# Optimization experiments

Hardware: AMD Instinct MI355X
Metric: run time of the kernel (lower is better)

Reference implementation:

```python
import jax, jax.numpy as jnp
import numpy as np

B, S, D, H = 2, 2048, 1024, 16
HD = D // H  # head dim = 64

def setup_inputs() -> dict:
    key = jax.random.key(0)
    ks = jax.random.split(key, 11)
    s = 0.02
    return {
        "query": jax.random.normal(ks[0], (B, S, D), jnp.float32),
        "key_in": jax.random.normal(ks[1], (B, S, D), jnp.float32),
        "value": jax.random.normal(ks[2], (B, S, D), jnp.float32),
        "Wq": jax.random.normal(ks[3], (D, D), jnp.float32) * s,
        "bq": jnp.zeros((D,), jnp.float32),
        "Wk": jax.random.normal(ks[4], (D, D), jnp.float32) * s,
        "bk": jnp.zeros((D,), jnp.float32),
        "Wv": jax.random.normal(ks[5], (D, D), jnp.float32) * s,
        "bv": jnp.zeros((D,), jnp.float32),
        "Wo": jax.random.normal(ks[6], (D, D), jnp.float32) * s,
        "bo": jnp.zeros((D,), jnp.float32),
    }

def _split_heads(x):
    b, s, _ = x.shape
    return x.reshape(b, s, H, HD).transpose(0, 2, 1, 3)  # [B,H,S,HD]

def reference(query, key_in, value, Wq, bq, Wk, bk, Wv, bv, Wo, bo):
    q = _split_heads(query @ Wq + bq)
    k = _split_heads(key_in @ Wk + bk)
    v = _split_heads(value @ Wv + bv)
    scores = jnp.einsum("bhqd,bhkd->bhqk", q, k) / jnp.sqrt(jnp.float32(HD))
    weights = jax.nn.softmax(scores, axis=-1)  # dropout = identity (eval)
    ctx = jnp.einsum("bhqk,bhkd->bhqd", weights, v)
    ctx = ctx.transpose(0, 2, 1, 3).reshape(query.shape[0], -1, D)
    return ctx @ Wo + bo
```

## Files before the change

kernel.cpp:

```cpp
#include <hip/hip_runtime.h>
#include <hip/hip_bf16.h>


typedef __attribute__((ext_vector_type(8))) short short8;
typedef __attribute__((ext_vector_type(4))) short short4v;
typedef __attribute__((ext_vector_type(4))) float f32x4;

static __device__ __forceinline__ short f2bf(float f) {
    union { float f; unsigned u; } c; c.f = f;
    unsigned r = c.u + 0x7fff + ((c.u >> 16) & 1);
    return (short)(r >> 16);
}

static __device__ __forceinline__ unsigned pk_bf16(float a, float b) {
    union { __hip_bfloat162 h; unsigned u; } c;
    c.h = __float22bfloat162_rn(make_float2(a, b));
    return c.u;
}

typedef const void __attribute__((address_space(1)))* gas_ptr;
typedef void __attribute__((address_space(3)))* las_ptr;
static __device__ __forceinline__ void gload16(const void* g, void* l) {
    __builtin_amdgcn_global_load_lds((gas_ptr)g, (las_ptr)l, 16, 0, 0);
}

__global__ __launch_bounds__(256) void prep(
    const float* __restrict__ X0, const float* __restrict__ X1,
    const float* __restrict__ X2, short* __restrict__ Abf,
    const float* __restrict__ W0, const float* __restrict__ W1,
    const float* __restrict__ W2, const float* __restrict__ W3,
    short* __restrict__ Wt)
{
    __shared__ float tile[32][33];
    const int bid = blockIdx.x;
    if (bid < 6144) {
        const int zz = bid >> 11, xb = bid & 2047;
        const float* X = zz == 0 ? X0 : zz == 1 ? X1 : X2;
        short* o = Abf + ((size_t)zz << 22);
        const int i = (xb * 256 + threadIdx.x) * 8;
        const float4 a = *(const float4*)(X + i);
        const float4 b = *(const float4*)(X + i + 4);
        uint4 r;
        r.x = pk_bf16(a.x, a.y); r.y = pk_bf16(a.z, a.w);
        r.z = pk_bf16(b.x, b.y); r.w = pk_bf16(b.z, b.w);
        *(uint4*)(o + i) = r;
    } else {
        const int wid = bid - 6144;
        const int z = wid >> 10;
        const float* W = z == 0 ? W0 : z == 1 ? W1 : z == 2 ? W2 : W3;
        short* O = Wt + ((size_t)z << 20);
        const int k0 = (wid & 31) * 32, n0 = ((wid >> 5) & 31) * 32;
        const int tx = threadIdx.x & 31, ty = threadIdx.x >> 5;
        #pragma unroll
        for (int j = 0; j < 32; j += 8)
            tile[ty + j][tx] = W[(k0 + ty + j) * 1024 + n0 + tx];
        __syncthreads();
        #pragma unroll
        for (int j = 0; j < 32; j += 8)
            O[(n0 + ty + j) * 1024 + k0 + tx] = f2bf(tile[tx][ty + j]);
    }
}

#define GEMM_CORE(Aa, Ba)                                                     \
    __shared__ short Al[2][2048];                           \
    __shared__ short Bl[2][4096];                          \
    const int t = threadIdx.x;                                                \
    const int m0 = blockIdx.y * 64, n0 = blockIdx.x * 128;                    \
    const int lane = t & 63, w = t >> 6;                                      \
    const int lm = lane & 15, lg = lane >> 4;                                 \
    const int wr = w >> 1, wc = w & 1;                                        \
    f32x4 acc[2][4] = {};                                                     \
    STAGE(0, 0);                                                              \
    __syncthreads();                                                          \
    int buf = 0;                                                              \
    for (int kk = 0; kk < 32; ++kk) {                                         \
        if (kk < 31) STAGE(buf ^ 1, (kk + 1) * 32);                           \
        const short* Ab = Al[buf];                                            \
        const short* Bb = Bl[buf];                                            \
        short8 af[2], bfr[4];                                                 \
        _Pragma("unroll")                                                     \
        for (int mf = 0; mf < 2; ++mf)                                        \
            af[mf] = *(const short8*)(Ab + (wr * 32 + mf * 16 + lm) * 32 + lg * 8); \
        _Pragma("unroll")                                                     \
        for (int nf = 0; nf < 4; ++nf)                                        \
            bfr[nf] = *(const short8*)(Bb + (wc * 64 + nf * 16 + lm) * 32 + lg * 8); \
        _Pragma("unroll")                                                     \
        for (int mf = 0; mf < 2; ++mf)                                        \
            _Pragma("unroll")                                                 \
            for (int nf = 0; nf < 4; ++nf)                                    \
                acc[mf][nf] = __builtin_amdgcn_mfma_f32_16x16x32_bf16(        \
                    af[mf], bfr[nf], acc[mf][nf], 0, 0, 0);                   \
        __syncthreads();                                                      \
        buf ^= 1;                                                             \
    }

#define STAGE(buf, k0) do {                                                   \
    gload16(Aa + (size_t)(m0 + (t >> 2)) * 1024 + (k0) + (t & 3) * 8,         \
            &Al[buf][w * 512]);                                               \
    _Pragma("unroll")                                                         \
    for (int j = 0; j < 2; ++j) {                                             \
        const int c = j * 256 + t;                                            \
        gload16(Ba + (size_t)(n0 + (c >> 2)) * 1024 + (k0) + (c & 3) * 8,     \
                &Bl[buf][j * 2048 + w * 512]);                                \
    }                                                                         \
} while (0)

__global__ __launch_bounds__(256) void gemmqkv(
    const short* __restrict__ Abase, const short* __restrict__ Wt,
    const float* __restrict__ bq, const float* __restrict__ bk,
    const float* __restrict__ bv, short* __restrict__ Qh,
    short* __restrict__ Kh, short* __restrict__ Vt, float qscale)
{
    const int z = blockIdx.z;
    const short* Aa = Abase + ((size_t)z << 22);
    const short* Ba = Wt + ((size_t)z << 20);
    const float* bias = z == 0 ? bq : z == 1 ? bk : bv;
    short* O = z == 0 ? Qh : z == 1 ? Kh : Vt;
    const float scale = z == 0 ? qscale : 1.0f;

    GEMM_CORE(Aa, Ba)

    #pragma unroll
    for (int mf = 0; mf < 2; ++mf) {
        const int mb = m0 + wr * 32 + mf * 16 + lg * 4;
        #pragma unroll
        for (int nf = 0; nf < 4; ++nf) {
            const int n = n0 + wc * 64 + nf * 16 + lm;
            const float bs = bias[n];
            if (z == 2) {
                short4v sv;
                #pragma unroll
                for (int i = 0; i < 4; ++i)
                    sv[i] = f2bf(acc[mf][nf][i] + bs);
                const int addr = (((mb >> 11) * 16 + (n >> 6)) * 64 + (n & 63)) * 2048 + (mb & 2047);
                *(short4v*)&O[addr] = sv;
            } else {
                #pragma unroll
                for (int i = 0; i < 4; ++i) {
                    const int m = mb + i;
                    const int addr = (((m >> 11) * 16 + (n >> 6)) * 2048 + (m & 2047)) * 64 + (n & 63);
                    O[addr] = f2bf(scale * (acc[mf][nf][i] + bs));
                }
            }
        }
    }
}

__global__ __launch_bounds__(256) void gemmo(
    const short* __restrict__ Aa, const short* __restrict__ Ba,
    const float* __restrict__ bias, float* __restrict__ Out)
{
    GEMM_CORE(Aa, Ba)

    #pragma unroll
    for (int mf = 0; mf < 2; ++mf) {
        const int mb = m0 + wr * 32 + mf * 16 + lg * 4;
        #pragma unroll
        for (int nf = 0; nf < 4; ++nf) {
            const int n = n0 + wc * 64 + nf * 16 + lm;
            const float bs = bias[n];
            #pragma unroll
            for (int i = 0; i < 4; ++i)
                Out[(mb + i) * 1024 + n] = acc[mf][nf][i] + bs;
        }
    }
}
#undef STAGE
#undef GEMM_CORE

__global__ __launch_bounds__(512, 4) void attn_k(
    const short* __restrict__ Q, const short* __restrict__ K,
    const short* __restrict__ V, short* __restrict__ Ctx)
{
    __shared__ short Kl[2][128][64];
    __shared__ short Vl[2][2][64][64];
    __shared__ short Pl[8][16][64];
    const int t = threadIdx.x;
    const int qt = blockIdx.x, bh = blockIdx.y;
    const int lane = t & 63, w = t >> 6;
    const int lm = lane & 15, lg = lane >> 4;
    const int swz = (lm & 7) << 3;
    const int swc = lm & 7;

    const int qrow = qt * 128 + w * 16 + lm;
    short8 qf[2];
    #pragma unroll
    for (int ks = 0; ks < 2; ++ks)
        qf[ks] = *(const short8*)(Q + ((size_t)bh * 2048 + qrow) * 64 + ks * 32 + lg * 8);

    float m_run = -3e38f, l_run = 0.f;
    f32x4 o_acc[4] = {};

    const int rk = t >> 2, ck = t & 3;
    const int rv = t >> 3, cv = t & 7;
    const short* Kg = K + ((size_t)bh * 2048 + rk) * 64 + ck * 16;
    const short* Vg = V + ((size_t)bh * 64 + rv) * 2048 + cv * 16;
    const int koff0 = rk * 64 + ((ck * 2) ^ (rk & 7)) * 8;
    const int koff1 = rk * 64 + ((ck * 2 + 1) ^ (rk & 7)) * 8;
    const int vhalf = (cv >> 2) * 4096;
    const int voff0 = vhalf + rv * 64 + (((cv * 2) & 7) ^ (rv & 7)) * 8;
    const int voff1 = vhalf + rv * 64 + (((cv * 2 + 1) & 7) ^ (rv & 7)) * 8;

    {
        short8 a = *(const short8*)(Kg);
        short8 b = *(const short8*)(Kg + 8);
        short8 c = *(const short8*)(Vg);
        short8 d = *(const short8*)(Vg + 8);
        *(short8*)((short*)Kl[0] + koff0) = a;
        *(short8*)((short*)Kl[0] + koff1) = b;
        *(short8*)((short*)Vl[0] + voff0) = c;
        *(short8*)((short*)Vl[0] + voff1) = d;
    }

    short* prow = &Pl[w][lm][0];
    int cur = 0;

    for (int kt = 0; kt < 16; ++kt) {
        __syncthreads();

        short8 kn0, kn1, vn0, vn1;
        const bool pfn = (kt < 15);
        if (pfn) {
            const short* Kgn = Kg + (size_t)(kt + 1) * 8192;
            const short* Vgn = Vg + (kt + 1) * 128;
            kn0 = *(const short8*)(Kgn);
            kn1 = *(const short8*)(Kgn + 8);
            vn0 = *(const short8*)(Vgn);
            vn1 = *(const short8*)(Vgn + 8);
        }

        const short* Kc = (const short*)Kl[cur];
        const short* Vc = (const short*)Vl[cur];

        f32x4 sa[2][4] = {};
        #pragma unroll
        for (int h = 0; h < 2; ++h)
            #pragma unroll
            for (int nf = 0; nf < 4; ++nf) {
                const int rr = h * 64 + nf * 16 + lm;
                #pragma unroll
                for (int ks = 0; ks < 2; ++ks) {
                    const short8 kf = *(const short8*)(Kc + rr * 64 + ((ks * 4 + lg) ^ swc) * 8);
                    sa[h][nf] = __builtin_amdgcn_mfma_f32_16x16x32_bf16(kf, qf[ks], sa[h][nf], 0, 0, 0);
                }
            }

        float mt = sa[0][0][0];
        #pragma unroll
        for (int h = 0; h < 2; ++h)
            #pragma unroll
            for (int nf = 0; nf < 4; ++nf)
                #pragma unroll
                for (int i = 0; i < 4; ++i)
                    mt = fmaxf(mt, sa[h][nf][i]);
        mt = fmaxf(mt, __shfl_xor(mt, 16));
        mt = fmaxf(mt, __shfl_xor(mt, 32));
        if (__any(mt > m_run + 8.0f)) {
            const float mn = fmaxf(m_run, mt);
            const float alpha = exp2f(m_run - mn);
            l_run *= alpha;
            #pragma unroll
            for (int nf = 0; nf < 4; ++nf)
                #pragma unroll
                for (int i = 0; i < 4; ++i)
                    o_acc[nf][i] *= alpha;
            m_run = mn;
        }
        float rs = 0.f;
        #pragma unroll
        for (int h = 0; h < 2; ++h)
            #pragma unroll
            for (int nf = 0; nf < 4; ++nf)
                #pragma unroll
                for (int i = 0; i < 4; ++i) {
                    const float e = exp2f(sa[h][nf][i] - m_run);
                    sa[h][nf][i] = e;
                    rs += e;
                }
        rs += __shfl_xor(rs, 16);
        rs += __shfl_xor(rs, 32);
        l_run += rs;

        #pragma unroll
        for (int h = 0; h < 2; ++h) {
            #pragma unroll
            for (int nf = 0; nf < 4; ++nf) {
                uint2 pv;
                pv.x = pk_bf16(sa[h][nf][0], sa[h][nf][1]);
                pv.y = pk_bf16(sa[h][nf][2], sa[h][nf][3]);
                *(uint2*)(prow + ((nf * 16 + lg * 4) ^ swz)) = pv;
            }
            short8 pf[2];
            #pragma unroll
            for (int ks = 0; ks < 2; ++ks)
                pf[ks] = *(const short8*)(prow + ((ks * 32 + lg * 8) ^ swz));

            if (h == 0 && pfn) {
                short* Kn = (short*)Kl[cur ^ 1];
                short* Vn = (short*)Vl[cur ^ 1];
                *(short8*)(Kn + koff0) = kn0;
                *(short8*)(Kn + koff1) = kn1;
                *(short8*)(Vn + voff0) = vn0;
                *(short8*)(Vn + voff1) = vn1;
            }

            #pragma unroll
            for (int nf = 0; nf < 4; ++nf) {
                const int rr = nf * 16 + lm;
                #pragma unroll
                for (int ks = 0; ks < 2; ++ks) {
                    const short8 vf = *(const short8*)(Vc + h * 4096 + rr * 64 + ((ks * 4 + lg) ^ swc) * 8);
                    o_acc[nf] = __builtin_amdgcn_mfma_f32_16x16x32_bf16(vf, pf[ks], o_acc[nf], 0, 0, 0);
                }
            }
        }
        cur ^= 1;
    }

    const float inv = 1.f / l_run;
    const int b = bh >> 4, h = bh & 15;
    short* outp = Ctx + ((size_t)b * 2048 + qrow) * 1024 + h * 64 + lg * 4;
    #pragma unroll
    for (int nf = 0; nf < 4; ++nf) {
        uint2 pk;
        pk.x = pk_bf16(o_acc[nf][0] * inv, o_acc[nf][1] * inv);
        pk.y = pk_bf16(o_acc[nf][2] * inv, o_acc[nf][3] * inv);
        *(uint2*)(outp + nf * 16) = pk;
    }
}

extern "C" void kernel_launch(void* const* d_in, const int* in_sizes, int n_in,
                              void* d_out, int out_size, void* d_ws, size_t ws_size,
                              hipStream_t stream)
{
    const float* query  = (const float*)d_in[0];
    const float* key_in = (const float*)d_in[1];
    const float* value  = (const float*)d_in[2];
    const float* Wq = (const float*)d_in[3];
    const float* bq = (const float*)d_in[4];
    const float* Wk = (const float*)d_in[5];
    const float* bk = (const float*)d_in[6];
    const float* Wv = (const float*)d_in[7];
    const float* bv = (const float*)d_in[8];
    const float* Wo = (const float*)d_in[9];
    const float* bo = (const float*)d_in[10];
    float* out = (float*)d_out;

    char* ws = (char*)d_ws;
    short* Wt  = (short*)(ws);
    short* Abf = (short*)(ws + (8  << 20));
    short* Qh  = (short*)(ws + (32 << 20));
    short* Kh  = (short*)(ws + (40 << 20));
    short* Vt  = (short*)(ws + (48 << 20));
    short* Ctx = Abf;

    const float qscale = 0.125f * 1.44269504088896f;

    hipLaunchKernelGGL(prep, dim3(10240), dim3(256), 0, stream,
                       query, key_in, value, Abf, Wq, Wk, Wv, Wo, Wt);
    hipLaunchKernelGGL(gemmqkv, dim3(8, 64, 3), dim3(256), 0, stream,
                       Abf, Wt, bq, bk, bv, Qh, Kh, Vt, qscale);
    hipLaunchKernelGGL(attn_k, dim3(16, 32), dim3(512), 0, stream,
                       Qh, Kh, Vt, Ctx);
    hipLaunchKernelGGL(gemmo, dim3(8, 64), dim3(256), 0, stream,
                       Ctx, Wt + (3 << 20), bo, out);
}
```

Before: 161.3 us.

## Fuse fp32-to-bf16 activation conversion into QKV GEMM loads; tree-reduce softmax max/sum

The separate prep pass that converted query/key/value to bf16 is removed. The QKV GEMM now loads fp32 activations straight into registers, converts them and writes swizzled bf16 into LDS after the MFMA work, which overlaps the global loads with compute. This removes a full write and re-read of 24MB of bf16 activations, but each GEMM block tile now reads fp32 A, and the A-tile rows are reread across the 8 N-blocks at twice the bytes. The attention softmax max and sum reductions are also rewritten as shallower trees to shorten dependency chains.

```diff
diff --git a/kernel.cpp b/kernel.cpp
--- a/kernel.cpp
+++ b/kernel.cpp
@@ -25,100 +25,113 @@
 }
 
 __global__ __launch_bounds__(256) void prep(
-    const float* __restrict__ X0, const float* __restrict__ X1,
-    const float* __restrict__ X2, short* __restrict__ Abf,
     const float* __restrict__ W0, const float* __restrict__ W1,
     const float* __restrict__ W2, const float* __restrict__ W3,
     short* __restrict__ Wt)
 {
     __shared__ float tile[32][33];
-    const int bid = blockIdx.x;
-    if (bid < 6144) {
-        const int zz = bid >> 11, xb = bid & 2047;
-        const float* X = zz == 0 ? X0 : zz == 1 ? X1 : X2;
-        short* o = Abf + ((size_t)zz << 22);
-        const int i = (xb * 256 + threadIdx.x) * 8;
-        const float4 a = *(const float4*)(X + i);
-        const float4 b = *(const float4*)(X + i + 4);
-        uint4 r;
-        r.x = pk_bf16(a.x, a.y); r.y = pk_bf16(a.z, a.w);
-        r.z = pk_bf16(b.x, b.y); r.w = pk_bf16(b.z, b.w);
-        *(uint4*)(o + i) = r;
-    } else {
-        const int wid = bid - 6144;
-        const int z = wid >> 10;
-        const float* W = z == 0 ? W0 : z == 1 ? W1 : z == 2 ? W2 : W3;
-        short* O = Wt + ((size_t)z << 20);
-        const int k0 = (wid & 31) * 32, n0 = ((wid >> 5) & 31) * 32;
-        const int tx = threadIdx.x & 31, ty = threadIdx.x >> 5;
-        #pragma unroll
-        for (int j = 0; j < 32; j += 8)
-            tile[ty + j][tx] = W[(k0 + ty + j) * 1024 + n0 + tx];
-        __syncthreads();
-        #pragma unroll
-        for (int j = 0; j < 32; j += 8)
-            O[(n0 + ty + j) * 1024 + k0 + tx] = f2bf(tile[tx][ty + j]);
-    }
-}
-
-#define GEMM_CORE(Aa, Ba)                                                     \
-    __shared__ short Al[2][2048];                           \
-    __shared__ short Bl[2][4096];                          \
-    const int t = threadIdx.x;                                                \
-    const int m0 = blockIdx.y * 64, n0 = blockIdx.x * 128;                    \
-    const int lane = t & 63, w = t >> 6;                                      \
-    const int lm = lane & 15, lg = lane >> 4;                                 \
-    const int wr = w >> 1, wc = w & 1;                                        \
-    f32x4 acc[2][4] = {};                                                     \
-    STAGE(0, 0);                                                              \
-    __syncthreads();                                                          \
-    int buf = 0;                                                              \
-    for (int kk = 0; kk < 32; ++kk) {                                         \
-        if (kk < 31) STAGE(buf ^ 1, (kk + 1) * 32);                           \
-        const short* Ab = Al[buf];                                            \
-        const short* Bb = Bl[buf];                                            \
-        short8 af[2], bfr[4];                                                 \
-        _Pragma("unroll")                                                     \
-        for (int mf = 0; mf < 2; ++mf)                                        \
-            af[mf] = *(const short8*)(Ab + (wr * 32 + mf * 16 + lm) * 32 + lg * 8); \
-        _Pragma("unroll")                                                     \
-        for (int nf = 0; nf < 4; ++nf)                                        \
-            bfr[nf] = *(const short8*)(Bb + (wc * 64 + nf * 16 + lm) * 32 + lg * 8); \
-        _Pragma("unroll")                                                     \
-        for (int mf = 0; mf < 2; ++mf)                                        \
-            _Pragma("unroll")                                                 \
-            for (int nf = 0; nf < 4; ++nf)                                    \
-                acc[mf][nf] = __builtin_amdgcn_mfma_f32_16x16x32_bf16(        \
-                    af[mf], bfr[nf], acc[mf][nf], 0, 0, 0);                   \
-        __syncthreads();                                                      \
-        buf ^= 1;                                                             \
-    }
-
-#define STAGE(buf, k0) do {                                                   \
-    gload16(Aa + (size_t)(m0 + (t >> 2)) * 1024 + (k0) + (t & 3) * 8,         \
-            &Al[buf][w * 512]);                                               \
-    _Pragma("unroll")                                                         \
-    for (int j = 0; j < 2; ++j) {                                             \
-        const int c = j * 256 + t;                                            \
-        gload16(Ba + (size_t)(n0 + (c >> 2)) * 1024 + (k0) + (c & 3) * 8,     \
-                &Bl[buf][j * 2048 + w * 512]);                                \
-    }                                                                         \
-} while (0)
+    const int wid = blockIdx.x;
+    const int z = wid >> 10;
+    const float* W = z == 0 ? W0 : z == 1 ? W1 : z == 2 ? W2 : W3;
+    short* O = Wt + ((size_t)z << 20);
+    const int k0 = (wid & 31) * 32, n0 = ((wid >> 5) & 31) * 32;
+    const int tx = threadIdx.x & 31, ty = threadIdx.x >> 5;
+    #pragma unroll
+    for (int j = 0; j < 32; j += 8)
+        tile[ty + j][tx] = W[(k0 + ty + j) * 1024 + n0 + tx];
+    __syncthreads();
+    #pragma unroll
+    for (int j = 0; j < 32; j += 8)
+        O[(n0 + ty + j) * 1024 + k0 + tx] = f2bf(tile[tx][ty + j]);
+}
 
 __global__ __launch_bounds__(256) void gemmqkv(
-    const short* __restrict__ Abase, const short* __restrict__ Wt,
+    const float* __restrict__ Xq, const float* __restrict__ Xk,
+    const float* __restrict__ Xv, const short* __restrict__ Wt,
     const float* __restrict__ bq, const float* __restrict__ bk,
     const float* __restrict__ bv, short* __restrict__ Qh,
     short* __restrict__ Kh, short* __restrict__ Vt, float qscale)
 {
+    __shared__ short Al[2][2048];
+    __shared__ short Bl[2][4096];
     const int z = blockIdx.z;
-    const short* Aa = Abase + ((size_t)z << 22);
+    const float* Af = z == 0 ? Xq : z == 1 ? Xk : Xv;
     const short* Ba = Wt + ((size_t)z << 20);
     const float* bias = z == 0 ? bq : z == 1 ? bk : bv;
     short* O = z == 0 ? Qh : z == 1 ? Kh : Vt;
     const float scale = z == 0 ? qscale : 1.0f;
 
-    GEMM_CORE(Aa, Ba)
+    const int t = threadIdx.x;
+    const int m0 = blockIdx.y * 64, n0 = blockIdx.x * 128;
+    const int lane = t & 63, w = t >> 6;
+    const int lm = lane & 15, lg = lane >> 4;
+    const int wr = w >> 1, wc = w & 1;
+
+    const int ar = t >> 2, ac = t & 3;
+    const int cw = ac ^ ((ar >> 1) & 3);
+    const float* Ag = Af + (size_t)(m0 + ar) * 1024 + ac * 8;
+    short* const adst0 = &Al[0][ar * 32 + cw * 8];
+    short* const adst1 = &Al[1][ar * 32 + cw * 8];
+    const int chA = lg ^ ((lm >> 1) & 3);
+
+    #define STAGEB(buf, k0) do {                                              \
+        _Pragma("unroll")                                                     \
+        for (int j = 0; j < 2; ++j) {                                         \
+            const int c = j * 256 + t;                                        \
+            gload16(Ba + (size_t)(n0 + (c >> 2)) * 1024 + (k0) + (c & 3) * 8, \
+                    &Bl[buf][j * 2048 + w * 512]);                            \
+        }                                                                     \
+    } while (0)
+    #define CVTA(dst, a0, a1) do {                                            \
+        uint4 wv_;                                                            \
+        wv_.x = pk_bf16((a0).x, (a0).y); wv_.y = pk_bf16((a0).z, (a0).w);     \
+        wv_.z = pk_bf16((a1).x, (a1).y); wv_.w = pk_bf16((a1).z, (a1).w);     \
+        *(uint4*)(dst) = wv_;                                                 \
+    } while (0)
+
+    f32x4 acc[2][4] = {};
+
+    {
+        float4 a0 = *(const float4*)(Ag);
+        float4 a1 = *(const float4*)(Ag + 4);
+        STAGEB(0, 0);
+        CVTA(adst0, a0, a1);
+    }
+    __syncthreads();
+
+    int buf = 0;
+    for (int kk = 0; kk < 32; ++kk) {
+        float4 a0, a1;
+        const bool pfn = (kk < 31);
+        if (pfn) {
+            const int kn = (kk + 1) * 32;
+            a0 = *(const float4*)(Ag + kn);
+            a1 = *(const float4*)(Ag + kn + 4);
+            STAGEB(buf ^ 1, kn);
+        }
+
+        const short* Ab = Al[buf];
+        const short* Bb = Bl[buf];
+        short8 af[2], bfr[4];
+        #pragma unroll
+        for (int mf = 0; mf < 2; ++mf)
+            af[mf] = *(const short8*)(Ab + (wr * 32 + mf * 16 + lm) * 32 + chA * 8);
+        #pragma unroll
+        for (int nf = 0; nf < 4; ++nf)
+            bfr[nf] = *(const short8*)(Bb + (wc * 64 + nf * 16 + lm) * 32 + lg * 8);
+        #pragma unroll
+        for (int mf = 0; mf < 2; ++mf)
+            #pragma unroll
+            for (int nf = 0; nf < 4; ++nf)
+                acc[mf][nf] = __builtin_amdgcn_mfma_f32_16x16x32_bf16(
+                    af[mf], bfr[nf], acc[mf][nf], 0, 0, 0);
+
+        if (pfn) CVTA(buf ? adst0 : adst1, a0, a1);
+        __syncthreads();
+        buf ^= 1;
+    }
+    #undef STAGEB
+    #undef CVTA
 
     #pragma unroll
     for (int mf = 0; mf < 2; ++mf) {
@@ -150,7 +163,50 @@
     const short* __restrict__ Aa, const short* __restrict__ Ba,
     const float* __restrict__ bias, float* __restrict__ Out)
 {
-    GEMM_CORE(Aa, Ba)
+    __shared__ short Al[2][2048];
+    __shared__ short Bl[2][4096];
+    const int t = threadIdx.x;
+    const int m0 = blockIdx.y * 64, n0 = blockIdx.x * 128;
+    const int lane = t & 63, w = t >> 6;
+    const int lm = lane & 15, lg = lane >> 4;
+    const int wr = w >> 1, wc = w & 1;
+
+    #define STAGE(buf, k0) do {                                               \
+        gload16(Aa + (size_t)(m0 + (t >> 2)) * 1024 + (k0) + (t & 3) * 8,     \
+                &Al[buf][w * 512]);                                           \
+        _Pragma("unroll")                                                     \
+        for (int j = 0; j < 2; ++j) {                                         \
+            const int c = j * 256 + t;                                        \
+            gload16(Ba + (size_t)(n0 + (c >> 2)) * 1024 + (k0) + (c & 3) * 8, \
+                    &Bl[buf][j * 2048 + w * 512]);                            \
+        }                                                                     \
+    } while (0)
+
+    f32x4 acc[2][4] = {};
+    STAGE(0, 0);
+    __syncthreads();
+    int buf = 0;
+    for (int kk = 0; kk < 32; ++kk) {
+        if (kk < 31) STAGE(buf ^ 1, (kk + 1) * 32);
+        const short* Ab = Al[buf];
+        const short* Bb = Bl[buf];
+        short8 af[2], bfr[4];
+        #pragma unroll
+        for (int mf = 0; mf < 2; ++mf)
+            af[mf] = *(const short8*)(Ab + (wr * 32 + mf * 16 + lm) * 32 + lg * 8);
+        #pragma unroll
+        for (int nf = 0; nf < 4; ++nf)
+            bfr[nf] = *(const short8*)(Bb + (wc * 64 + nf * 16 + lm) * 32 + lg * 8);
+        #pragma unroll
+        for (int mf = 0; mf < 2; ++mf)
+            #pragma unroll
+            for (int nf = 0; nf < 4; ++nf)
+                acc[mf][nf] = __builtin_amdgcn_mfma_f32_16x16x32_bf16(
+                    af[mf], bfr[nf], acc[mf][nf], 0, 0, 0);
+        __syncthreads();
+        buf ^= 1;
+    }
+    #undef STAGE
 
     #pragma unroll
     for (int mf = 0; mf < 2; ++mf) {
@@ -165,8 +221,6 @@
         }
     }
 }
-#undef STAGE
-#undef GEMM_CORE
 
 __global__ __launch_bounds__(512, 4) void attn_k(
     const short* __restrict__ Q, const short* __restrict__ K,
@@ -245,14 +299,16 @@
                 }
             }
 
-        float mt = sa[0][0][0];
+        float mx[8];
         #pragma unroll
         for (int h = 0; h < 2; ++h)
             #pragma unroll
-            for (int nf = 0; nf < 4; ++nf)
-                #pragma unroll
-                for (int i = 0; i < 4; ++i)
-                    mt = fmaxf(mt, sa[h][nf][i]);
+            for (int nf = 0; nf < 4; ++nf) {
+                const f32x4 v = sa[h][nf];
+                mx[h * 4 + nf] = fmaxf(fmaxf(v[0], v[1]), fmaxf(v[2], v[3]));
+            }
+        float mt = fmaxf(fmaxf(fmaxf(mx[0], mx[1]), fmaxf(mx[2], mx[3])),
+                         fmaxf(fmaxf(mx[4], mx[5]), fmaxf(mx[6], mx[7])));
         mt = fmaxf(mt, __shfl_xor(mt, 16));
         mt = fmaxf(mt, __shfl_xor(mt, 32));
         if (__any(mt > m_run + 8.0f)) {
@@ -266,17 +322,19 @@
                     o_acc[nf][i] *= alpha;
             m_run = mn;
         }
-        float rs = 0.f;
+        float ps[8];
         #pragma unroll
         for (int h = 0; h < 2; ++h)
             #pragma unroll
-            for (int nf = 0; nf < 4; ++nf)
-                #pragma unroll
-                for (int i = 0; i < 4; ++i) {
-                    const float e = exp2f(sa[h][nf][i] - m_run);
-                    sa[h][nf][i] = e;
-                    rs += e;
-                }
+            for (int nf = 0; nf < 4; ++nf) {
+                f32x4 v = sa[h][nf];
+                #pragma unroll
+                for (int i = 0; i < 4; ++i) v[i] = exp2f(v[i] - m_run);
+                sa[h][nf] = v;
+                ps[h * 4 + nf] = (v[0] + v[1]) + (v[2] + v[3]);
+            }
+        float rs = ((ps[0] + ps[1]) + (ps[2] + ps[3])) +
+                   ((ps[4] + ps[5]) + (ps[6] + ps[7]));
         rs += __shfl_xor(rs, 16);
         rs += __shfl_xor(rs, 32);
         l_run += rs;
@@ -348,18 +406,17 @@
 
     char* ws = (char*)d_ws;
     short* Wt  = (short*)(ws);
-    short* Abf = (short*)(ws + (8  << 20));
+    short* Ctx = (short*)(ws + (8  << 20));
     short* Qh  = (short*)(ws + (32 << 20));
     short* Kh  = (short*)(ws + (40 << 20));
     short* Vt  = (short*)(ws + (48 << 20));
-    short* Ctx = Abf;
 
     const float qscale = 0.125f * 1.44269504088896f;
 
-    hipLaunchKernelGGL(prep, dim3(10240), dim3(256), 0, stream,
-                       query, key_in, value, Abf, Wq, Wk, Wv, Wo, Wt);
+    hipLaunchKernelGGL(prep, dim3(4096), dim3(256), 0, stream,
+                       Wq, Wk, Wv, Wo, Wt);
     hipLaunchKernelGGL(gemmqkv, dim3(8, 64, 3), dim3(256), 0, stream,
-                       Abf, Wt, bq, bk, bv, Qh, Kh, Vt, qscale);
+                       query, key_in, value, Wt, bq, bk, bv, Qh, Kh, Vt, qscale);
     hipLaunchKernelGGL(attn_k, dim3(16, 32), dim3(512), 0, stream,
                        Qh, Kh, Vt, Ctx);
     hipLaunchKernelGGL(gemmo, dim3(8, 64), dim3(256), 0, stream,
```

Measured after the change: 166.1 us. +3.0%, slower.
